# Optimization experiments

Hardware: AMD Instinct MI355X
Metric: run time of the kernel (lower is better)

## Reference

```python
import jax, jax.numpy as jnp
import numpy as np

N0, N1 = 81, 319          # hard-coded split t1[:, :81] / t1[:, 81:]
C_OUT = 64
LAYERS = 5
EPS = 1e-5


def _temporal_conv(X, w1, b1, wc, bc):
    # X: [B, N, T, Cin] -> NCHW with H=N, W=T, kernel (1, 3), VALID
    out_ch = w1.shape[0]
    Xp = jnp.transpose(X, (0, 3, 1, 2))
    dn = ('NCHW', 'OIHW', 'NCHW')
    conv = lambda x, w: jax.lax.conv_general_dilated(x, w, (1, 1), 'VALID', dimension_numbers=dn)
    xc = conv(Xp, wc) + bc[None, :, None, None]
    temp = conv(Xp, w1) + b1[None, :, None, None]
    x_p, x_q = xc[:, :out_ch], xc[:, out_ch:]
    out = (x_p + temp) * jax.nn.sigmoid(x_q)
    return jnp.transpose(out, (0, 2, 3, 1))  # [B, N, T-2, out_ch]


def _het_conv(X0l, X1l, X00, Aaa, Aab, Aba, th1, th2, th3):
    # torch einsum('ij,jklm->kilm', A, X.permute(1,0,2,3)) == einsum('ij,bjtc->bitc', A, X)
    u1 = jnp.einsum('ij,bjtc->bitc', Aaa, X0l)
    u2 = jax.nn.relu(u1 @ th1)
    u3 = jnp.einsum('ij,bjtc->bitc', Aab @ Aba, X0l)
    u4 = jnp.einsum('ij,bjtc->bitc', Aab, X1l)
    u5 = jax.nn.sigmoid(u3 @ th2 + u4 @ th3)
    u6 = jax.nn.relu((u2 + u5) * 0.5)
    return jax.nn.relu(0.9 * u6 + 0.1 * X00)


def setup_inputs() -> dict:
    key = jax.random.key(0)
    ks = jax.random.split(key, 24)
    B, N, T, Cin = 16, 400, 32, 2
    stdv = 1.0 / np.sqrt(C_OUT)
    u = lambda k, shape, s: jax.random.uniform(k, shape, jnp.float32, -s, s)
    inp = {
        'X': jax.random.normal(ks[0], (B, N, T, Cin), jnp.float32),
        'A00': jax.random.uniform(ks[1], (N0, N0), jnp.float32) / N0,
        'A01': jax.random.uniform(ks[2], (N0, N1), jnp.float32) / N1,
        'A10': jax.random.uniform(ks[3], (N1, N0), jnp.float32) / N0,
        'A11': jax.random.uniform(ks[4], (N1, N1), jnp.float32) / N1,
        't1_conv1_w': jax.random.normal(ks[5], (C_OUT, Cin, 1, 3), jnp.float32) * 0.1,
        't1_conv1_b': jnp.zeros((C_OUT,), jnp.float32),
        't1_causal_w': jax.random.normal(ks[6], (2 * C_OUT, Cin, 1, 3), jnp.float32) * 0.1,
        't1_causal_b': jnp.zeros((2 * C_OUT,), jnp.float32),
        'g1_th1': u(ks[7], (LAYERS, C_OUT, C_OUT), stdv),
        'g1_th2': u(ks[8], (LAYERS, C_OUT, C_OUT), stdv),
        'g1_th3': u(ks[9], (LAYERS, C_OUT, C_OUT), stdv),
        'g2_th1': u(ks[10], (LAYERS, C_OUT, C_OUT), stdv),
        'g2_th2': u(ks[11], (LAYERS, C_OUT, C_OUT), stdv),
        'g2_th3': u(ks[12], (LAYERS, C_OUT, C_OUT), stdv),
        'theta': u(ks[13], (C_OUT, C_OUT), stdv),
        't2_conv1_w': jax.random.normal(ks[14], (C_OUT, C_OUT, 1, 3), jnp.float32) * 0.05,
        't2_conv1_b': jnp.zeros((C_OUT,), jnp.float32),
        't2_causal_w': jax.random.normal(ks[15], (2 * C_OUT, C_OUT, 1, 3), jnp.float32) * 0.05,
        't2_causal_b': jnp.zeros((2 * C_OUT,), jnp.float32),
        'bn_gamma': jnp.ones((N,), jnp.float32),
        'bn_beta': jnp.zeros((N,), jnp.float32),
    }
    return inp


def reference(X, A00, A01, A10, A11, t1_conv1_w, t1_conv1_b, t1_causal_w, t1_causal_b,
              g1_th1, g1_th2, g1_th3, g2_th1, g2_th2, g2_th3, theta,
              t2_conv1_w, t2_conv1_b, t2_causal_w, t2_causal_b, bn_gamma, bn_beta):
    t1 = _temporal_conv(X, t1_conv1_w, t1_conv1_b, t1_causal_w, t1_causal_b)  # [B,N,T-2,64]
    X0, X1 = t1[:, :N0], t1[:, N0:]
    u0, u1v = X0, X1
    for i in range(LAYERS):
        u0 = _het_conv(u0, u1v, X0, A00, A01, A10, g1_th1[i], g1_th2[i], g1_th3[i])
        u1v = _het_conv(u1v, u0, X1, A11, A10, A01, g2_th1[i], g2_th2[i], g2_th3[i])
    tk = jnp.concatenate([u0, u1v], axis=1)            # [B,N,T-2,64]
    tk = jax.nn.relu(tk @ theta)
    tk = _temporal_conv(tk, t2_conv1_w, t2_conv1_b, t2_causal_w, t2_causal_b)  # [B,N,T-4,64]
    # BatchNorm2d(num_nodes): channel axis is the node axis (dim 1), training-mode batch stats
    mean = tk.mean(axis=(0, 2, 3), keepdims=True)
    var = tk.var(axis=(0, 2, 3), keepdims=True)
    return (tk - mean) / jnp.sqrt(var + EPS) * bn_gamma[None, :, None, None] + bn_beta[None, :, None, None]
```

## Files before the change

kernel.cpp:

```cpp
#include <hip/hip_runtime.h>


typedef __attribute__((ext_vector_type(8))) short short8v;
typedef __attribute__((ext_vector_type(4))) short short4v;
typedef __attribute__((ext_vector_type(4))) float f32x4;

#define BB 16
#define NA 81
#define NB 319
#define PA 128
#define PB 320
#define M1 1920
#define T1 30
#define T2 28

#define MFMA16 __builtin_amdgcn_mfma_f32_16x16x32_bf16

__device__ __forceinline__ float sigmoidf_(float x){ return 1.0f/(1.0f+__expf(-x)); }
__device__ __forceinline__ short f2bf(float f){
  unsigned u = __float_as_uint(f);
  u += 0x7FFF + ((u>>16)&1);
  return (short)(u>>16);
}
__device__ __forceinline__ float bf2f(short s){
  return __uint_as_float(((unsigned)(unsigned short)s)<<16);
}

__global__ __launch_bounds__(256) void k_prep_mm(const float* __restrict__ A01,
                                                 const float* __restrict__ A10,
                                                 float* __restrict__ Ma,
                                                 float* __restrict__ Mb) {
  int idx = blockIdx.x*256 + threadIdx.x;
  if (idx < NA*NA) {
    int i = idx / NA, j = idx % NA;
    float a = 0.f;
    for (int k = 0; k < NB; ++k) a += A01[i*NB + k]*A10[k*NA + j];
    Ma[idx] = a;
  } else {
    idx -= NA*NA;
    if (idx >= NB*NB) return;
    int i = idx / NB, j = idx % NB;
    float a = 0.f;
    for (int k = 0; k < NA; ++k) a += A10[i*NA + k]*A01[k*NB + j];
    Mb[idx] = a;
  }
}

__device__ __forceinline__ void packA_one(int f, const float* src, int I, int J,
                                          int ld, int nIt, short* dst) {
  int e = f & 7, l = (f >> 3) & 63, rest = f >> 9;
  int it = rest % nIt, jt = rest / nIt;
  int i = it*16 + (l & 15);
  int j = jt*32 + (l >> 4)*8 + e;
  float v = (i < I && j < J) ? src[i*ld + j] : 0.f;
  dst[f] = f2bf(v);
}

__global__ __launch_bounds__(256) void k_pack_A(
    const float* __restrict__ A00, const float* __restrict__ A01,
    const float* __restrict__ A10, const float* __restrict__ A11,
    const float* __restrict__ Ma, const float* __restrict__ Mb,
    short* __restrict__ A00pk, short* __restrict__ Mapk,
    short* __restrict__ A01pk, short* __restrict__ A10pk,
    short* __restrict__ A11pk, short* __restrict__ Mbpk) {
  int idx = blockIdx.x*256 + threadIdx.x;
  if (idx < 12288)        { packA_one(idx, A00, NA, NA, NA, 8,  A00pk); return; }
  idx -= 12288;
  if (idx < 12288)        { packA_one(idx, Ma,  NA, NA, NA, 8,  Mapk);  return; }
  idx -= 12288;
  if (idx < 40960)        { packA_one(idx, A01, NA, NB, NB, 8,  A01pk); return; }
  idx -= 40960;
  if (idx < 30720)        { packA_one(idx, A10, NB, NA, NA, 20, A10pk); return; }
  idx -= 30720;
  if (idx < 102400)       { packA_one(idx, A11, NB, NB, NB, 20, A11pk); return; }
  idx -= 102400;
  if (idx < 102400)       { packA_one(idx, Mb,  NB, NB, NB, 20, Mbpk);  return; }
}

__global__ __launch_bounds__(256) void k_pack_th(
    const float* __restrict__ g1t1, const float* __restrict__ g1t2,
    const float* __restrict__ g1t3, const float* __restrict__ g2t1,
    const float* __restrict__ g2t2, const float* __restrict__ g2t3,
    const float* __restrict__ theta,
    const float* __restrict__ w12, const float* __restrict__ wc2,
    const float* __restrict__ w11, const float* __restrict__ wc1,
    const float* __restrict__ b11, const float* __restrict__ bc1,
    short* __restrict__ thpk, short* __restrict__ thetapk,
    short* __restrict__ W2pk, float* __restrict__ W1t, float* __restrict__ B1t) {
  int idx = blockIdx.x*256 + threadIdx.x;
  if (idx < 122880) {
    int mat = idx / 4096, rem = idx % 4096;
    int ct = rem / 1024, ks = (rem / 512) & 1, l = (rem >> 3) & 63, e = rem & 7;
    int ci = ks*32 + (l >> 4)*8 + e, co = ct*16 + (l & 15);
    int layer = mat / 6, which = mat % 6;
    const float* src = which == 0 ? g1t1 : which == 1 ? g1t2 : which == 2 ? g1t3
                     : which == 3 ? g2t1 : which == 4 ? g2t2 : g2t3;
    thpk[idx] = f2bf(src[layer*4096 + ci*64 + co]);
    return;
  }
  idx -= 122880;
  if (idx < 4096) {
    int ct = idx / 1024, ks = (idx / 512) & 1, l = (idx >> 3) & 63, e = idx & 7;
    int ci = ks*32 + (l >> 4)*8 + e, co = ct*16 + (l & 15);
    thetapk[idx] = f2bf(theta[ci*64 + co]);
    return;
  }
  idx -= 4096;
  if (idx < 36864) {
    int ct = idx / 3072, rem = idx % 3072;
    int ks = rem / 512, l = (rem >> 3) & 63, e = rem & 7;
    int kap = ks*32 + (l >> 4)*8 + e;
    int k = kap >> 6, ci = kap & 63;
    int cc = ct*16 + (l & 15);
    float v = (cc < 64) ? w12[cc*192 + ci*3 + k] : wc2[(cc - 64)*192 + ci*3 + k];
    W2pk[idx] = f2bf(v);
    return;
  }
  idx -= 36864;
  if (idx < 1152) {
    int kk = idx / 192, cc = idx % 192;
    int k = kk >> 1, ci = kk & 1;
    W1t[idx] = (cc < 64) ? w11[cc*6 + ci*3 + k] : wc1[(cc - 64)*6 + ci*3 + k];
    return;
  }
  idx -= 1152;
  if (idx < 192) { B1t[idx] = (idx < 64) ? b11[idx] : bc1[idx - 64]; return; }
}

__global__ __launch_bounds__(192) void k_tconv1(const float* __restrict__ X,
                                                const float* __restrict__ W1t,
                                                const float* __restrict__ B1t,
                                                short* __restrict__ t1a,
                                                short* __restrict__ t1b) {
  __shared__ float xl[64];
  __shared__ float wl[6*192];
  __shared__ float bl[192];
  __shared__ float ol[T1*192];
  int bn = blockIdx.x;
  int b = bn / 400, n = bn % 400;
  int tid = threadIdx.x;
  if (tid < 64) xl[tid] = X[(size_t)bn*64 + tid];
  for (int i2 = tid; i2 < 6*192; i2 += 192) wl[i2] = W1t[i2];
  bl[tid] = B1t[tid];
  __syncthreads();
  float acc[T1];
  float bias = bl[tid];
#pragma unroll
  for (int t = 0; t < T1; ++t) acc[t] = bias;
#pragma unroll
  for (int kk = 0; kk < 6; ++kk) {
    float w = wl[kk*192 + tid];
    int k = kk >> 1, ci = kk & 1;
#pragma unroll
    for (int t = 0; t < T1; ++t) acc[t] += xl[(t + k)*2 + ci]*w;
  }
#pragma unroll
  for (int t = 0; t < T1; ++t) ol[t*192 + tid] = acc[t];
  __syncthreads();
  short* dst = (n < NA) ? (t1a + ((size_t)b*PA + n)*M1)
                        : (t1b + ((size_t)b*PB + (n - NA))*M1);
  for (int p = tid; p < T1*64; p += 192) {
    int t = p >> 6, c = p & 63;
    float v = (ol[t*192 + 64 + c] + ol[t*192 + c])*sigmoidf_(ol[t*192 + 128 + c]);
    dst[p] = f2bf(v);
  }
}

__global__ __launch_bounds__(256) void k_transpose(const short* __restrict__ src,
                                                   short* __restrict__ dst, int Ipad) {
  int lane = threadIdx.x & 63, wv = threadIdx.x >> 6;
  int n = blockIdx.x*64 + lane;
  int b = blockIdx.z;
  const short* sp = src + ((size_t)b*Ipad + n)*M1;
  int mbase = (blockIdx.y*4 + wv)*120;
  for (int k = 0; k < 120; k += 8) {
    int m = mbase + k;
    short8v v = *(const short8v*)(sp + m);
#pragma unroll
    for (int e = 0; e < 8; ++e)
      dst[((size_t)b*M1 + m + e)*Ipad + n] = v[e];
  }
}

template<int KT12, int KT3>
__global__ __launch_bounds__(128, 1) void k_layer(
    const short* __restrict__ XT12, int Jp12,
    const short* __restrict__ XT3, int Jp3,
    const short* __restrict__ Apk1, const short* __restrict__ Apk2, int nIt12,
    const short* __restrict__ Apk3, int nIt3,
    const short* __restrict__ th1, const short* __restrict__ th2,
    const short* __restrict__ th3,
    const short* __restrict__ X00, short* __restrict__ uout,
    short* __restrict__ umT, int NW, int I, int IpadO) {
  __shared__ short sd[2][3][32*68];
  int lane = threadIdx.x & 63, wv = threadIdx.x >> 6;
  int ln = lane & 15, qw = lane >> 4;

  int total = NW*15*BB;
  int d = blockIdx.x;
  int logical = (d & 7)*(total >> 3) + (d >> 3);
  int w = logical % NW;
  int rest = logical / NW;
  int mt = rest % 15;
  int b = rest / 15;

  int m0 = (mt*2 + wv)*64;
  int t = m0 >> 6;

  short* s1 = sd[wv][0];
  short* s2 = sd[wv][1];
  short* s3 = sd[wv][2];

  short8v x0r[4];
#pragma unroll
  for (int kq = 0; kq < 4; ++kq) {
    int il = kq*8 + (lane >> 3);
    int irow = w*32 + il;
    if (irow >= I) irow = I - 1;
    size_t ro = ((size_t)b*IpadO + irow)*M1 + t*64 + (lane & 7)*8;
    x0r[kq] = *(const short8v*)(X00 + ro);
  }

  {
    f32x4 a3[2][4];
#pragma unroll
    for (int ft = 0; ft < 2; ++ft)
#pragma unroll
      for (int mf = 0; mf < 4; ++mf) a3[ft][mf] = (f32x4)0.f;

    short8v xa[2][4];
    short8v b3f[2][2];
#pragma unroll
    for (int mf = 0; mf < 4; ++mf) {
      size_t ro = ((size_t)b*M1 + m0 + mf*16 + ln)*Jp3 + qw*8;
      xa[0][mf] = *(const short8v*)(XT3 + ro);
    }
    {
      size_t ab = (((size_t)0*nIt3 + w*2)*64 + lane)*8;
      b3f[0][0] = *(const short8v*)(Apk3 + ab);
      b3f[0][1] = *(const short8v*)(Apk3 + ab + 512);
    }
#pragma unroll
    for (int ks = 0; ks < KT3; ++ks) {
      if (ks + 1 < KT3) {
        int nx = (ks + 1) & 1;
#pragma unroll
        for (int mf = 0; mf < 4; ++mf) {
          size_t ro = ((size_t)b*M1 + m0 + mf*16 + ln)*Jp3 + (ks + 1)*32 + qw*8;
          xa[nx][mf] = *(const short8v*)(XT3 + ro);
        }
        size_t ab = (((size_t)(ks + 1)*nIt3 + w*2)*64 + lane)*8;
        b3f[nx][0] = *(const short8v*)(Apk3 + ab);
        b3f[nx][1] = *(const short8v*)(Apk3 + ab + 512);
      }
      int cu = ks & 1;
#pragma unroll
      for (int mf = 0; mf < 4; ++mf) {
        a3[0][mf] = MFMA16(xa[cu][mf], b3f[cu][0], a3[0][mf], 0, 0, 0);
        a3[1][mf] = MFMA16(xa[cu][mf], b3f[cu][1], a3[1][mf], 0, 0, 0);
      }
    }
#pragma unroll
    for (int ft = 0; ft < 2; ++ft)
#pragma unroll
      for (int mf = 0; mf < 4; ++mf) {
        int irow = ft*16 + ln;
        int cc = mf*16 + qw*4;
        short4v v3;
#pragma unroll
        for (int r = 0; r < 4; ++r) v3[r] = f2bf(a3[ft][mf][r]);
        *(short4v*)(s3 + irow*68 + cc) = v3;
      }
  }

  {
    f32x4 a1[2][4], a2[2][4];
#pragma unroll
    for (int ft = 0; ft < 2; ++ft)
#pragma unroll
      for (int mf = 0; mf < 4; ++mf) { a1[ft][mf] = (f32x4)0.f; a2[ft][mf] = (f32x4)0.f; }

    short8v xa[2][4];
    short8v b1f[2][2], b2f[2][2];
#pragma unroll
    for (int mf = 0; mf < 4; ++mf) {
      size_t ro = ((size_t)b*M1 + m0 + mf*16 + ln)*Jp12 + qw*8;
      xa[0][mf] = *(const short8v*)(XT12 + ro);
    }
    {
      size_t ab = (((size_t)0*nIt12 + w*2)*64 + lane)*8;
      b1f[0][0] = *(const short8v*)(Apk1 + ab);
      b1f[0][1] = *(const short8v*)(Apk1 + ab + 512);
      b2f[0][0] = *(const short8v*)(Apk2 + ab);
      b2f[0][1] = *(const short8v*)(Apk2 + ab + 512);
    }
#pragma unroll
    for (int ks = 0; ks < KT12; ++ks) {
      if (ks + 1 < KT12) {
        int nx = (ks + 1) & 1;
#pragma unroll
        for (int mf = 0; mf < 4; ++mf) {
          size_t ro = ((size_t)b*M1 + m0 + mf*16 + ln)*Jp12 + (ks + 1)*32 + qw*8;
          xa[nx][mf] = *(const short8v*)(XT12 + ro);
        }
        size_t ab = (((size_t)(ks + 1)*nIt12 + w*2)*64 + lane)*8;
        b1f[nx][0] = *(const short8v*)(Apk1 + ab);
        b1f[nx][1] = *(const short8v*)(Apk1 + ab + 512);
        b2f[nx][0] = *(const short8v*)(Apk2 + ab);
        b2f[nx][1] = *(const short8v*)(Apk2 + ab + 512);
      }
      int cu = ks & 1;
#pragma unroll
      for (int mf = 0; mf < 4; ++mf) {
        a1[0][mf] = MFMA16(xa[cu][mf], b1f[cu][0], a1[0][mf], 0, 0, 0);
        a1[1][mf] = MFMA16(xa[cu][mf], b1f[cu][1], a1[1][mf], 0, 0, 0);
        a2[0][mf] = MFMA16(xa[cu][mf], b2f[cu][0], a2[0][mf], 0, 0, 0);
        a2[1][mf] = MFMA16(xa[cu][mf], b2f[cu][1], a2[1][mf], 0, 0, 0);
      }
    }
#pragma unroll
    for (int ft = 0; ft < 2; ++ft)
#pragma unroll
      for (int mf = 0; mf < 4; ++mf) {
        int irow = ft*16 + ln;
        int cc = mf*16 + qw*4;
        short4v v1, v2;
#pragma unroll
        for (int r = 0; r < 4; ++r) {
          v1[r] = f2bf(a1[ft][mf][r]);
          v2[r] = f2bf(a2[ft][mf][r]);
        }
        *(short4v*)(s1 + irow*68 + cc) = v1;
        *(short4v*)(s2 + irow*68 + cc) = v2;
      }
  }

  f32x4 u2a[2][4], u5a[2][4];
#pragma unroll
  for (int fi = 0; fi < 2; ++fi)
#pragma unroll
    for (int ct = 0; ct < 4; ++ct) { u2a[fi][ct] = (f32x4)0.f; u5a[fi][ct] = (f32x4)0.f; }

#pragma unroll
  for (int ks = 0; ks < 2; ++ks) {
    short8v f1[2], f2[2], f3[2];
#pragma unroll
    for (int fi = 0; fi < 2; ++fi) {
      int irow = fi*16 + ln;
      f1[fi] = *(const short8v*)(s1 + irow*68 + ks*32 + qw*8);
      f2[fi] = *(const short8v*)(s2 + irow*68 + ks*32 + qw*8);
      f3[fi] = *(const short8v*)(s3 + irow*68 + ks*32 + qw*8);
    }
#pragma unroll
    for (int ct = 0; ct < 4; ++ct) {
      short8v b1 = *(const short8v*)(th1 + ((ct*2 + ks)*64 + lane)*8);
      short8v b2 = *(const short8v*)(th2 + ((ct*2 + ks)*64 + lane)*8);
      short8v b3 = *(const short8v*)(th3 + ((ct*2 + ks)*64 + lane)*8);
#pragma unroll
      for (int fi = 0; fi < 2; ++fi) {
        u2a[fi][ct] = MFMA16(f1[fi], b1, u2a[fi][ct], 0, 0, 0);
        u5a[fi][ct] = MFMA16(f2[fi], b2, u5a[fi][ct], 0, 0, 0);
        u5a[fi][ct] = MFMA16(f3[fi], b3, u5a[fi][ct], 0, 0, 0);
      }
    }
  }

#pragma unroll
  for (int kq = 0; kq < 4; ++kq) {
    int il = kq*8 + (lane >> 3);
    *(short8v*)(s3 + il*68 + (lane & 7)*8) = x0r[kq];
  }

  short* sg = s1;
#pragma unroll
  for (int fi = 0; fi < 2; ++fi)
#pragma unroll
    for (int ct = 0; ct < 4; ++ct) {
      int co = ct*16 + ln;
#pragma unroll
      for (int r = 0; r < 4; ++r) {
        int il = fi*16 + qw*4 + r;
        int i = w*32 + il;
        short g = 0;
        if (i < I) {
          float u2 = fmaxf(u2a[fi][ct][r], 0.f);
          float u5 = sigmoidf_(u5a[fi][ct][r]);
          float u6 = fmaxf(0.5f*(u2 + u5), 0.f);
          float x0 = bf2f(s3[il*68 + co]);
          g = f2bf(fmaxf(0.9f*u6 + 0.1f*x0, 0.f));
        }
        sg[il*68 + co] = g;
      }
    }

#pragma unroll
  for (int kq = 0; kq < 4; ++kq) {
    int il = kq*8 + (lane >> 3);
    int irow = w*32 + il;
    short8v v = *(const short8v*)(sg + il*68 + (lane & 7)*8);
    if (irow < I)
      *(short8v*)(uout + ((size_t)b*IpadO + irow)*M1 + t*64 + (lane & 7)*8) = v;
  }

  {
    int co = lane;
    size_t cb = ((size_t)b*M1 + t*64 + co)*IpadO + w*32;
#pragma unroll
    for (int kq = 0; kq < 4; ++kq) {
      short8v v;
#pragma unroll
      for (int ii = 0; ii < 8; ++ii) v[ii] = sg[(kq*8 + ii)*68 + co];
      *(short8v*)(umT + cb + kq*8) = v;
    }
  }
}

__global__ __launch_bounds__(256) void k_thconv2(const short* __restrict__ u0,
                                                 const short* __restrict__ u1,
                                                 const short* __restrict__ thetapk,
                                                 const short* __restrict__ W2pk,
                                                 const float* __restrict__ b12,
                                                 const float* __restrict__ bc2,
                                                 float* __restrict__ out) {
  __shared__ short lds[34*72];
  int tid = threadIdx.x, lane = tid & 63, wv = tid >> 6;
  int ln = lane & 15, qw = lane >> 4;
  int bn = blockIdx.x;
  int b = blockIdx.y;
  const short* u; int i, Ipad;
  if (bn < NA) { u = u0; i = bn; Ipad = PA; }
  else         { u = u1; i = bn - NA; Ipad = PB; }
  for (int z = tid; z < 4*72; z += 256) lds[30*72 + z] = 0;

  f32x4 ac[2];
  ac[0] = (f32x4)0.f; ac[1] = (f32x4)0.f;
  size_t ubase = ((size_t)b*Ipad + i)*M1;
#pragma unroll
  for (int ks = 0; ks < 2; ++ks) {
    short8v bm = *(const short8v*)(thetapk + ((wv*2 + ks)*64 + lane)*8);
#pragma unroll
    for (int tf = 0; tf < 2; ++tf) {
      short8v af = *(const short8v*)(u + ubase + (tf*16 + ln)*64 + ks*32 + qw*8);
      ac[tf] = MFMA16(af, bm, ac[tf], 0, 0, 0);
    }
  }
#pragma unroll
  for (int tf = 0; tf < 2; ++tf)
#pragma unroll
    for (int r = 0; r < 4; ++r) {
      int t = tf*16 + qw*4 + r;
      if (t < T1) lds[t*72 + wv*16 + ln] = f2bf(fmaxf(ac[tf][r], 0.f));
    }
  __syncthreads();

  f32x4 a3[2][3];
#pragma unroll
  for (int tf = 0; tf < 2; ++tf)
#pragma unroll
    for (int s = 0; s < 3; ++s) a3[tf][s] = (f32x4)0.f;
  for (int ks = 0; ks < 6; ++ks) {
    short8v af[2];
#pragma unroll
    for (int tf = 0; tf < 2; ++tf) {
      int m = (tf*16 + ln)*64 + ks*32 + qw*8;
      af[tf] = *(const short8v*)(lds + (m >> 6)*72 + (m & 63));
    }
#pragma unroll
    for (int s = 0; s < 3; ++s) {
      int ct = wv + s*4;
      short8v bm = *(const short8v*)(W2pk + ((ct*6 + ks)*64 + lane)*8);
#pragma unroll
      for (int tf = 0; tf < 2; ++tf)
        a3[tf][s] = MFMA16(af[tf], bm, a3[tf][s], 0, 0, 0);
    }
  }
  int co = wv*16 + ln;
  float btm = b12[co], bp = bc2[co], bq = bc2[64 + co];
#pragma unroll
  for (int tf = 0; tf < 2; ++tf)
#pragma unroll
    for (int r = 0; r < 4; ++r) {
      int t = tf*16 + qw*4 + r;
      if (t >= T2) continue;
      float tm = a3[tf][0][r] + btm;
      float p  = a3[tf][1][r] + bp;
      float q  = a3[tf][2][r] + bq;
      out[((size_t)(b*400 + bn)*T2 + t)*64 + co] = (p + tm)*sigmoidf_(q);
    }
}

__global__ __launch_bounds__(256) void k_bn_stats(const float* __restrict__ y,
                                                  float* __restrict__ stats) {
  int n = blockIdx.x;
  int tid = threadIdx.x;
  float s = 0.f, ss = 0.f;
  for (int b = 0; b < BB; ++b) {
    const float* p = y + ((size_t)(b*400 + n))*(T2*64);
    for (int i2 = tid; i2 < T2*64; i2 += 256) {
      float v = p[i2];
      s += v; ss += v*v;
    }
  }
  __shared__ float rs[4], rss[4];
  for (int off = 32; off > 0; off >>= 1) {
    s += __shfl_down(s, off);
    ss += __shfl_down(ss, off);
  }
  if ((tid & 63) == 0) { rs[tid >> 6] = s; rss[tid >> 6] = ss; }
  __syncthreads();
  if (tid == 0) {
    float S = rs[0] + rs[1] + rs[2] + rs[3];
    float SS = rss[0] + rss[1] + rss[2] + rss[3];
    float mean = S/28672.f;
    float var = SS/28672.f - mean*mean;
    stats[n] = mean;
    stats[400 + n] = rsqrtf(var + 1e-5f);
  }
}

__global__ void k_bn_apply(float* __restrict__ y, const float* __restrict__ stats,
                           const float* __restrict__ gamma, const float* __restrict__ beta) {
  int idx = blockIdx.x*blockDim.x + threadIdx.x;
  const int total = BB*400*T2*64/4;
  for (; idx < total; idx += gridDim.x*blockDim.x) {
    int e = idx*4;
    int n = (e/(T2*64)) % 400;
    float mean = stats[n];
    float g = gamma[n]*stats[400 + n];
    float bt = beta[n];
    float4 v = ((float4*)y)[idx];
    v.x = (v.x - mean)*g + bt;
    v.y = (v.y - mean)*g + bt;
    v.z = (v.z - mean)*g + bt;
    v.w = (v.w - mean)*g + bt;
    ((float4*)y)[idx] = v;
  }
}

extern "C" void kernel_launch(void* const* d_in, const int* in_sizes, int n_in,
                              void* d_out, int out_size, void* d_ws, size_t ws_size,
                              hipStream_t stream) {
  const float* X     = (const float*)d_in[0];
  const float* A00   = (const float*)d_in[1];
  const float* A01   = (const float*)d_in[2];
  const float* A10   = (const float*)d_in[3];
  const float* A11   = (const float*)d_in[4];
  const float* w11   = (const float*)d_in[5];
  const float* b11   = (const float*)d_in[6];
  const float* wc1   = (const float*)d_in[7];
  const float* bc1   = (const float*)d_in[8];
  const float* g1t1  = (const float*)d_in[9];
  const float* g1t2  = (const float*)d_in[10];
  const float* g1t3  = (const float*)d_in[11];
  const float* g2t1  = (const float*)d_in[12];
  const float* g2t2  = (const float*)d_in[13];
  const float* g2t3  = (const float*)d_in[14];
  const float* theta = (const float*)d_in[15];
  const float* w12   = (const float*)d_in[16];
  const float* b12   = (const float*)d_in[17];
  const float* wc2   = (const float*)d_in[18];
  const float* bc2   = (const float*)d_in[19];
  const float* gamma = (const float*)d_in[20];
  const float* beta  = (const float*)d_in[21];

  short* ws = (short*)d_ws;
  size_t o = 0;
  const size_t szA = (size_t)BB*PA*M1;
  const size_t szB = (size_t)BB*PB*M1;
  short* t1a  = ws + o; o += szA;
  short* t1b  = ws + o; o += szB;
  short* u0   = ws + o; o += szA;
  short* u1   = ws + o; o += szB;
  short* uaT0 = ws + o; o += szA;
  short* uaT1 = ws + o; o += szA;
  short* ubT0 = ws + o; o += szB;
  short* ubT1 = ws + o; o += szB;
  short* A00pk = ws + o; o += 12288;
  short* Mapk  = ws + o; o += 12288;
  short* A01pk = ws + o; o += 40960;
  short* A10pk = ws + o; o += 30720;
  short* A11pk = ws + o; o += 102400;
  short* Mbpk  = ws + o; o += 102400;
  short* thpk    = ws + o; o += 122880;
  short* thetapk = ws + o; o += 4096;
  short* W2pk    = ws + o; o += 36864;
  o = (o + 7) & ~(size_t)7;
  float* fws = (float*)(ws + o);
  float* Ma    = fws;
  float* Mb    = Ma + 6561;
  float* stats = Mb + 101761;
  float* W1t   = stats + 800;
  float* B1t   = W1t + 1152;

  k_prep_mm<<<424, 256, 0, stream>>>(A01, A10, Ma, Mb);
  k_pack_A<<<1176, 256, 0, stream>>>(A00, A01, A10, A11, Ma, Mb,
                                     A00pk, Mapk, A01pk, A10pk, A11pk, Mbpk);
  k_pack_th<<<646, 256, 0, stream>>>(g1t1, g1t2, g1t3, g2t1, g2t2, g2t3, theta,
                                     w12, wc2, w11, wc1, b11, bc1,
                                     thpk, thetapk, W2pk, W1t, B1t);
  k_tconv1<<<BB*400, 192, 0, stream>>>(X, W1t, B1t, t1a, t1b);
  k_transpose<<<dim3(PA/64, 4, BB), 256, 0, stream>>>(t1a, uaT0, PA);
  k_transpose<<<dim3(PB/64, 4, BB), 256, 0, stream>>>(t1b, ubT0, PB);

  short* uaT[2] = {uaT0, uaT1};
  short* ubT[2] = {ubT0, ubT1};
  for (int l = 0; l < 5; ++l) {
    int pin = l & 1, pout = 1 - pin;
    const short* th = thpk + (size_t)(l*6)*4096;
    k_layer<3, 10><<<720, 128, 0, stream>>>(
        uaT[pin], PA, ubT[pin], PB, A00pk, Mapk, 8, A01pk, 8,
        th + 0*4096, th + 1*4096, th + 2*4096, t1a, u0, uaT[pout], 3, NA, PA);
    k_layer<10, 3><<<2400, 128, 0, stream>>>(
        ubT[pin], PB, uaT[pout], PA, A11pk, Mbpk, 20, A10pk, 20,
        th + 3*4096, th + 4*4096, th + 5*4096, t1b, u1, ubT[pout], 10, NB, PB);
  }

  k_thconv2<<<dim3(400, BB), 256, 0, stream>>>(u0, u1, thetapk, W2pk, b12, bc2,
                                               (float*)d_out);
  k_bn_stats<<<400, 256, 0, stream>>>((float*)d_out, stats);
  k_bn_apply<<<2048, 256, 0, stream>>>((float*)d_out, stats, gamma, beta);
}
```

Baseline: 538.9 us.

## Reassociate A10·A01·X1 via intermediate from layer-a to avoid 319x319 product

Drops the precomputed Mb = A10·A01 (319x319) and instead computes A10·(A01·X1) by reusing the A01·X1 intermediate that layer A already produces, which is now written out transposed to a new g3T buffer. Layer B becomes a specialized kernel whose Mb contraction (K=10 tiles) shrinks to a K=3 contraction over the 81-node side, shared with the A10·u0 term. This removes the large Mb prep and pack work and cuts MFMA work in layer B, at the cost of extra global writes and reads of g3T and different bf16 rounding of the intermediate.

```diff
diff --git a/kernel.cpp b/kernel.cpp
--- a/kernel.cpp
+++ b/kernel.cpp
@@ -28,22 +28,13 @@
 
 __global__ __launch_bounds__(256) void k_prep_mm(const float* __restrict__ A01,
                                                  const float* __restrict__ A10,
-                                                 float* __restrict__ Ma,
-                                                 float* __restrict__ Mb) {
+                                                 float* __restrict__ Ma) {
   int idx = blockIdx.x*256 + threadIdx.x;
-  if (idx < NA*NA) {
-    int i = idx / NA, j = idx % NA;
-    float a = 0.f;
-    for (int k = 0; k < NB; ++k) a += A01[i*NB + k]*A10[k*NA + j];
-    Ma[idx] = a;
-  } else {
-    idx -= NA*NA;
-    if (idx >= NB*NB) return;
-    int i = idx / NB, j = idx % NB;
-    float a = 0.f;
-    for (int k = 0; k < NA; ++k) a += A10[i*NA + k]*A01[k*NB + j];
-    Mb[idx] = a;
-  }
+  if (idx >= NA*NA) return;
+  int i = idx / NA, j = idx % NA;
+  float a = 0.f;
+  for (int k = 0; k < NB; ++k) a += A01[i*NB + k]*A10[k*NA + j];
+  Ma[idx] = a;
 }
 
 __device__ __forceinline__ void packA_one(int f, const float* src, int I, int J,
@@ -59,10 +50,10 @@
 __global__ __launch_bounds__(256) void k_pack_A(
     const float* __restrict__ A00, const float* __restrict__ A01,
     const float* __restrict__ A10, const float* __restrict__ A11,
-    const float* __restrict__ Ma, const float* __restrict__ Mb,
+    const float* __restrict__ Ma,
     short* __restrict__ A00pk, short* __restrict__ Mapk,
     short* __restrict__ A01pk, short* __restrict__ A10pk,
-    short* __restrict__ A11pk, short* __restrict__ Mbpk) {
+    short* __restrict__ A11pk) {
   int idx = blockIdx.x*256 + threadIdx.x;
   if (idx < 12288)        { packA_one(idx, A00, NA, NA, NA, 8,  A00pk); return; }
   idx -= 12288;
@@ -73,8 +64,6 @@
   if (idx < 30720)        { packA_one(idx, A10, NB, NA, NA, 20, A10pk); return; }
   idx -= 30720;
   if (idx < 102400)       { packA_one(idx, A11, NB, NB, NB, 20, A11pk); return; }
-  idx -= 102400;
-  if (idx < 102400)       { packA_one(idx, Mb,  NB, NB, NB, 20, Mbpk);  return; }
 }
 
 __global__ __launch_bounds__(256) void k_pack_th(
@@ -183,7 +172,7 @@
 }
 
 template<int KT12, int KT3>
-__global__ __launch_bounds__(128, 1) void k_layer(
+__global__ __launch_bounds__(128, 1) void k_layer_a(
     const short* __restrict__ XT12, int Jp12,
     const short* __restrict__ XT3, int Jp3,
     const short* __restrict__ Apk1, const short* __restrict__ Apk2, int nIt12,
@@ -191,7 +180,8 @@
     const short* __restrict__ th1, const short* __restrict__ th2,
     const short* __restrict__ th3,
     const short* __restrict__ X00, short* __restrict__ uout,
-    short* __restrict__ umT, int NW, int I, int IpadO) {
+    short* __restrict__ umT, short* __restrict__ g3T,
+    int NW, int I, int IpadO) {
   __shared__ short sd[2][3][32*68];
   int lane = threadIdx.x & 63, wv = threadIdx.x >> 6;
   int ln = lane & 15, qw = lane >> 4;
@@ -271,6 +261,17 @@
         for (int r = 0; r < 4; ++r) v3[r] = f2bf(a3[ft][mf][r]);
         *(short4v*)(s3 + irow*68 + cc) = v3;
       }
+  }
+  {
+    int co = lane;
+    size_t cb = ((size_t)b*M1 + t*64 + co)*IpadO + w*32;
+#pragma unroll
+    for (int kq = 0; kq < 4; ++kq) {
+      short8v v;
+#pragma unroll
+      for (int ii = 0; ii < 8; ++ii) v[ii] = s3[(kq*8 + ii)*68 + co];
+      *(short8v*)(g3T + cb + kq*8) = v;
+    }
   }
 
   {
@@ -332,6 +333,238 @@
         }
         *(short4v*)(s1 + irow*68 + cc) = v1;
         *(short4v*)(s2 + irow*68 + cc) = v2;
+      }
+  }
+
+  f32x4 u2a[2][4], u5a[2][4];
+#pragma unroll
+  for (int fi = 0; fi < 2; ++fi)
+#pragma unroll
+    for (int ct = 0; ct < 4; ++ct) { u2a[fi][ct] = (f32x4)0.f; u5a[fi][ct] = (f32x4)0.f; }
+
+#pragma unroll
+  for (int ks = 0; ks < 2; ++ks) {
+    short8v f1[2], f2[2], f3[2];
+#pragma unroll
+    for (int fi = 0; fi < 2; ++fi) {
+      int irow = fi*16 + ln;
+      f1[fi] = *(const short8v*)(s1 + irow*68 + ks*32 + qw*8);
+      f2[fi] = *(const short8v*)(s2 + irow*68 + ks*32 + qw*8);
+      f3[fi] = *(const short8v*)(s3 + irow*68 + ks*32 + qw*8);
+    }
+#pragma unroll
+    for (int ct = 0; ct < 4; ++ct) {
+      short8v b1 = *(const short8v*)(th1 + ((ct*2 + ks)*64 + lane)*8);
+      short8v b2 = *(const short8v*)(th2 + ((ct*2 + ks)*64 + lane)*8);
+      short8v b3 = *(const short8v*)(th3 + ((ct*2 + ks)*64 + lane)*8);
+#pragma unroll
+      for (int fi = 0; fi < 2; ++fi) {
+        u2a[fi][ct] = MFMA16(f1[fi], b1, u2a[fi][ct], 0, 0, 0);
+        u5a[fi][ct] = MFMA16(f2[fi], b2, u5a[fi][ct], 0, 0, 0);
+        u5a[fi][ct] = MFMA16(f3[fi], b3, u5a[fi][ct], 0, 0, 0);
+      }
+    }
+  }
+
+#pragma unroll
+  for (int kq = 0; kq < 4; ++kq) {
+    int il = kq*8 + (lane >> 3);
+    *(short8v*)(s3 + il*68 + (lane & 7)*8) = x0r[kq];
+  }
+
+  short* sg = s1;
+#pragma unroll
+  for (int fi = 0; fi < 2; ++fi)
+#pragma unroll
+    for (int ct = 0; ct < 4; ++ct) {
+      int co = ct*16 + ln;
+#pragma unroll
+      for (int r = 0; r < 4; ++r) {
+        int il = fi*16 + qw*4 + r;
+        int i = w*32 + il;
+        short g = 0;
+        if (i < I) {
+          float u2 = fmaxf(u2a[fi][ct][r], 0.f);
+          float u5 = sigmoidf_(u5a[fi][ct][r]);
+          float u6 = fmaxf(0.5f*(u2 + u5), 0.f);
+          float x0 = bf2f(s3[il*68 + co]);
+          g = f2bf(fmaxf(0.9f*u6 + 0.1f*x0, 0.f));
+        }
+        sg[il*68 + co] = g;
+      }
+    }
+
+#pragma unroll
+  for (int kq = 0; kq < 4; ++kq) {
+    int il = kq*8 + (lane >> 3);
+    int irow = w*32 + il;
+    short8v v = *(const short8v*)(sg + il*68 + (lane & 7)*8);
+    if (irow < I)
+      *(short8v*)(uout + ((size_t)b*IpadO + irow)*M1 + t*64 + (lane & 7)*8) = v;
+  }
+
+  {
+    int co = lane;
+    size_t cb = ((size_t)b*M1 + t*64 + co)*IpadO + w*32;
+#pragma unroll
+    for (int kq = 0; kq < 4; ++kq) {
+      short8v v;
+#pragma unroll
+      for (int ii = 0; ii < 8; ++ii) v[ii] = sg[(kq*8 + ii)*68 + co];
+      *(short8v*)(umT + cb + kq*8) = v;
+    }
+  }
+}
+
+__global__ __launch_bounds__(128, 1) void k_layer_b(
+    const short* __restrict__ X2T,
+    const short* __restrict__ X3T,
+    const short* __restrict__ X1T,
+    const short* __restrict__ ApkS,
+    const short* __restrict__ Apk1,
+    const short* __restrict__ th1, const short* __restrict__ th2,
+    const short* __restrict__ th3,
+    const short* __restrict__ X00, short* __restrict__ uout,
+    short* __restrict__ umT) {
+  const int NW = 10, I = NB, IpadO = PB;
+  __shared__ short sd[2][3][32*68];
+  int lane = threadIdx.x & 63, wv = threadIdx.x >> 6;
+  int ln = lane & 15, qw = lane >> 4;
+
+  int total = NW*15*BB;
+  int d = blockIdx.x;
+  int logical = (d & 7)*(total >> 3) + (d >> 3);
+  int w = logical % NW;
+  int rest = logical / NW;
+  int mt = rest % 15;
+  int b = rest / 15;
+
+  int m0 = (mt*2 + wv)*64;
+  int t = m0 >> 6;
+
+  short* s1 = sd[wv][0];
+  short* s2 = sd[wv][1];
+  short* s3 = sd[wv][2];
+
+  short8v x0r[4];
+#pragma unroll
+  for (int kq = 0; kq < 4; ++kq) {
+    int il = kq*8 + (lane >> 3);
+    int irow = w*32 + il;
+    if (irow >= I) irow = I - 1;
+    size_t ro = ((size_t)b*IpadO + irow)*M1 + t*64 + (lane & 7)*8;
+    x0r[kq] = *(const short8v*)(X00 + ro);
+  }
+
+  {
+    f32x4 a2[2][4], a3[2][4];
+#pragma unroll
+    for (int ft = 0; ft < 2; ++ft)
+#pragma unroll
+      for (int mf = 0; mf < 4; ++mf) { a2[ft][mf] = (f32x4)0.f; a3[ft][mf] = (f32x4)0.f; }
+
+    short8v x2[2][4], x3[2][4];
+    short8v bf[2][2];
+#pragma unroll
+    for (int mf = 0; mf < 4; ++mf) {
+      size_t ro = ((size_t)b*M1 + m0 + mf*16 + ln)*PA + qw*8;
+      x2[0][mf] = *(const short8v*)(X2T + ro);
+      x3[0][mf] = *(const short8v*)(X3T + ro);
+    }
+    {
+      size_t ab = (((size_t)0*20 + w*2)*64 + lane)*8;
+      bf[0][0] = *(const short8v*)(ApkS + ab);
+      bf[0][1] = *(const short8v*)(ApkS + ab + 512);
+    }
+#pragma unroll
+    for (int ks = 0; ks < 3; ++ks) {
+      if (ks + 1 < 3) {
+        int nx = (ks + 1) & 1;
+#pragma unroll
+        for (int mf = 0; mf < 4; ++mf) {
+          size_t ro = ((size_t)b*M1 + m0 + mf*16 + ln)*PA + (ks + 1)*32 + qw*8;
+          x2[nx][mf] = *(const short8v*)(X2T + ro);
+          x3[nx][mf] = *(const short8v*)(X3T + ro);
+        }
+        size_t ab = (((size_t)(ks + 1)*20 + w*2)*64 + lane)*8;
+        bf[nx][0] = *(const short8v*)(ApkS + ab);
+        bf[nx][1] = *(const short8v*)(ApkS + ab + 512);
+      }
+      int cu = ks & 1;
+#pragma unroll
+      for (int mf = 0; mf < 4; ++mf) {
+        a2[0][mf] = MFMA16(x2[cu][mf], bf[cu][0], a2[0][mf], 0, 0, 0);
+        a2[1][mf] = MFMA16(x2[cu][mf], bf[cu][1], a2[1][mf], 0, 0, 0);
+        a3[0][mf] = MFMA16(x3[cu][mf], bf[cu][0], a3[0][mf], 0, 0, 0);
+        a3[1][mf] = MFMA16(x3[cu][mf], bf[cu][1], a3[1][mf], 0, 0, 0);
+      }
+    }
+#pragma unroll
+    for (int ft = 0; ft < 2; ++ft)
+#pragma unroll
+      for (int mf = 0; mf < 4; ++mf) {
+        int irow = ft*16 + ln;
+        int cc = mf*16 + qw*4;
+        short4v v2, v3;
+#pragma unroll
+        for (int r = 0; r < 4; ++r) {
+          v2[r] = f2bf(a2[ft][mf][r]);
+          v3[r] = f2bf(a3[ft][mf][r]);
+        }
+        *(short4v*)(s2 + irow*68 + cc) = v2;
+        *(short4v*)(s3 + irow*68 + cc) = v3;
+      }
+  }
+
+  {
+    f32x4 a1[2][4];
+#pragma unroll
+    for (int ft = 0; ft < 2; ++ft)
+#pragma unroll
+      for (int mf = 0; mf < 4; ++mf) a1[ft][mf] = (f32x4)0.f;
+
+    short8v xa[2][4];
+    short8v b1f[2][2];
+#pragma unroll
+    for (int mf = 0; mf < 4; ++mf) {
+      size_t ro = ((size_t)b*M1 + m0 + mf*16 + ln)*PB + qw*8;
+      xa[0][mf] = *(const short8v*)(X1T + ro);
+    }
+    {
+      size_t ab = (((size_t)0*20 + w*2)*64 + lane)*8;
+      b1f[0][0] = *(const short8v*)(Apk1 + ab);
+      b1f[0][1] = *(const short8v*)(Apk1 + ab + 512);
+    }
+#pragma unroll
+    for (int ks = 0; ks < 10; ++ks) {
+      if (ks + 1 < 10) {
+        int nx = (ks + 1) & 1;
+#pragma unroll
+        for (int mf = 0; mf < 4; ++mf) {
+          size_t ro = ((size_t)b*M1 + m0 + mf*16 + ln)*PB + (ks + 1)*32 + qw*8;
+          xa[nx][mf] = *(const short8v*)(X1T + ro);
+        }
+        size_t ab = (((size_t)(ks + 1)*20 + w*2)*64 + lane)*8;
+        b1f[nx][0] = *(const short8v*)(Apk1 + ab);
+        b1f[nx][1] = *(const short8v*)(Apk1 + ab + 512);
+      }
+      int cu = ks & 1;
+#pragma unroll
+      for (int mf = 0; mf < 4; ++mf) {
+        a1[0][mf] = MFMA16(xa[cu][mf], b1f[cu][0], a1[0][mf], 0, 0, 0);
+        a1[1][mf] = MFMA16(xa[cu][mf], b1f[cu][1], a1[1][mf], 0, 0, 0);
+      }
+    }
+#pragma unroll
+    for (int ft = 0; ft < 2; ++ft)
+#pragma unroll
+      for (int mf = 0; mf < 4; ++mf) {
+        int irow = ft*16 + ln;
+        int cc = mf*16 + qw*4;
+        short4v v1;
+#pragma unroll
+        for (int r = 0; r < 4; ++r) v1[r] = f2bf(a1[ft][mf][r]);
+        *(short4v*)(s1 + irow*68 + cc) = v1;
       }
   }
 
@@ -575,26 +808,25 @@
   short* uaT1 = ws + o; o += szA;
   short* ubT0 = ws + o; o += szB;
   short* ubT1 = ws + o; o += szB;
+  short* g3T  = ws + o; o += szA;
   short* A00pk = ws + o; o += 12288;
   short* Mapk  = ws + o; o += 12288;
   short* A01pk = ws + o; o += 40960;
   short* A10pk = ws + o; o += 30720;
   short* A11pk = ws + o; o += 102400;
-  short* Mbpk  = ws + o; o += 102400;
   short* thpk    = ws + o; o += 122880;
   short* thetapk = ws + o; o += 4096;
   short* W2pk    = ws + o; o += 36864;
   o = (o + 7) & ~(size_t)7;
   float* fws = (float*)(ws + o);
   float* Ma    = fws;
-  float* Mb    = Ma + 6561;
-  float* stats = Mb + 101761;
+  float* stats = Ma + 6561;
   float* W1t   = stats + 800;
   float* B1t   = W1t + 1152;
 
-  k_prep_mm<<<424, 256, 0, stream>>>(A01, A10, Ma, Mb);
-  k_pack_A<<<1176, 256, 0, stream>>>(A00, A01, A10, A11, Ma, Mb,
-                                     A00pk, Mapk, A01pk, A10pk, A11pk, Mbpk);
+  k_prep_mm<<<26, 256, 0, stream>>>(A01, A10, Ma);
+  k_pack_A<<<776, 256, 0, stream>>>(A00, A01, A10, A11, Ma,
+                                    A00pk, Mapk, A01pk, A10pk, A11pk);
   k_pack_th<<<646, 256, 0, stream>>>(g1t1, g1t2, g1t3, g2t1, g2t2, g2t3, theta,
                                      w12, wc2, w11, wc1, b11, bc1,
                                      thpk, thetapk, W2pk, W1t, B1t);
@@ -607,12 +839,13 @@
   for (int l = 0; l < 5; ++l) {
     int pin = l & 1, pout = 1 - pin;
     const short* th = thpk + (size_t)(l*6)*4096;
-    k_layer<3, 10><<<720, 128, 0, stream>>>(
+    k_layer_a<3, 10><<<720, 128, 0, stream>>>(
         uaT[pin], PA, ubT[pin], PB, A00pk, Mapk, 8, A01pk, 8,
-        th + 0*4096, th + 1*4096, th + 2*4096, t1a, u0, uaT[pout], 3, NA, PA);
-    k_layer<10, 3><<<2400, 128, 0, stream>>>(
-        ubT[pin], PB, uaT[pout], PA, A11pk, Mbpk, 20, A10pk, 20,
-        th + 3*4096, th + 4*4096, th + 5*4096, t1b, u1, ubT[pout], 10, NB, PB);
+        th + 0*4096, th + 1*4096, th + 2*4096, t1a, u0, uaT[pout], g3T,
+        3, NA, PA);
+    k_layer_b<<<2400, 128, 0, stream>>>(
+        g3T, uaT[pout], ubT[pin], A10pk, A11pk,
+        th + 3*4096, th + 4*4096, th + 5*4096, t1b, u1, ubT[pout]);
   }
 
   k_thconv2<<<dim3(400, BB), 256, 0, stream>>>(u0, u1, thetapk, W2pk, b12, bc2,
```

Result: no change. 537.0 us (-0.3%).
